# Optimization experiments

Measured on AMD Instinct MI355X. Metric: run time of the kernel, lower is better.

## Reference

```python
import math
import jax, jax.numpy as jnp
import numpy as np

N_NODES = 100000
N_EDGES = 1600000
IN_DIM = 512
HID = 128
OUT_DIM = 1
N_LAYERS = 8
ALPHA = 0.1
THETA = 0.5


def setup_inputs() -> dict:
    key = jax.random.key(0)
    ks = jax.random.split(key, 8)
    x = jax.random.normal(ks[0], (N_NODES, IN_DIM), dtype=jnp.float32)
    edge_index = jax.random.randint(ks[1], (2, N_EDGES), 0, N_NODES, dtype=jnp.int64)
    edge_weight = jax.random.uniform(ks[2], (N_EDGES,), dtype=jnp.float32)
    s_in = 1.0 / math.sqrt(IN_DIM)
    s_h = 1.0 / math.sqrt(HID)
    W_in = jax.random.uniform(ks[3], (IN_DIM, HID), jnp.float32, -s_in, s_in)
    b_in = jax.random.uniform(ks[4], (HID,), jnp.float32, -s_in, s_in)
    W_layers = jax.random.uniform(ks[5], (N_LAYERS, HID, HID), jnp.float32, -s_h, s_h)
    W_out = jax.random.uniform(ks[6], (HID, OUT_DIM), jnp.float32, -s_h, s_h)
    b_out = jax.random.uniform(ks[7], (OUT_DIM,), jnp.float32, -s_h, s_h)
    return {"x": x, "edge_index": edge_index, "edge_weight": edge_weight,
            "W_in": W_in, "b_in": b_in, "W_layers": W_layers,
            "W_out": W_out, "b_out": b_out}


def _gcn_norm(edge_index, n_nodes, dtype):
    # gcn_norm with add_self_loops=True and unit edge weights
    # (GCN2Net never forwards edge_weight into GCN2Conv).
    loop = jnp.arange(n_nodes, dtype=edge_index.dtype)
    src = jnp.concatenate([edge_index[0], loop])
    dst = jnp.concatenate([edge_index[1], loop])
    w = jnp.ones(src.shape[0], dtype=dtype)
    deg = jax.ops.segment_sum(w, dst, num_segments=n_nodes)
    dinv = jnp.where(deg > 0, jax.lax.rsqrt(deg), 0.0).astype(dtype)
    norm = dinv[src] * w * dinv[dst]
    return src, dst, norm


def reference(x, edge_index, edge_weight, W_in, b_in, W_layers, W_out, b_out):
    n = x.shape[0]
    src, dst, norm = _gcn_norm(edge_index, n, x.dtype)

    x = x @ W_in + b_in          # initial_proj: [N, HID]
    x0 = x
    for i in range(N_LAYERS):
        # sparse neighbor aggregation: A_hat @ x
        agg = jax.ops.segment_sum(x[src] * norm[:, None], dst, num_segments=n)
        # initial residual
        h = (1.0 - ALPHA) * agg + ALPHA * x0
        # identity mapping (shared_weights=True): (1-beta)*h + beta*(h @ W)
        beta = math.log(THETA / (i + 1) + 1.0)
        x = (1.0 - beta) * h + beta * (h @ W_layers[i])
        x = jax.nn.relu(x)
        # dropout omitted (eval mode / drop_prob=0)
    return x @ W_out + b_out     # final_proj: [N, OUT_DIM]
```

## Files before the change

### kernel.cpp

```cpp
#include <hip/hip_runtime.h>
#include <math.h>

#define NN 100000
#define NE 1600000
#define IN_DIM 512
#define HID 128
#define N_LAYERS 8
#define NB 98
#define PADMAX 2000000
#define NBUCK 391
#define BCAP2 4608
#define EPB 4096

typedef __attribute__((ext_vector_type(4))) float f32x4;
typedef __attribute__((ext_vector_type(8))) _Float16 h16x8;
typedef __attribute__((ext_vector_type(2))) _Float16 h16x2;


__global__ void deg_count_kernel(const int* __restrict__ dst, int* __restrict__ deg) {
    int e = blockIdx.x * blockDim.x + threadIdx.x;
    if (e < NE) atomicAdd(&deg[dst[e]], 1);
}

__global__ void dinv_kernel(const int* __restrict__ deg, float* __restrict__ dinv) {
    int i = blockIdx.x * blockDim.x + threadIdx.x;
    if (i < NN) dinv[i] = rsqrtf((float)(deg[i] + 1));
}

__global__ void scan1_kernel(const int* __restrict__ deg, int* __restrict__ bsum) {
    __shared__ int s[16];
    int gi = blockIdx.x * 1024 + threadIdx.x;
    int d = (gi < NN) ? deg[gi] : 0;
    int r = (d + 3) & ~3;
    for (int off = 32; off; off >>= 1) r += __shfl_down(r, off, 64);
    if ((threadIdx.x & 63) == 0) s[threadIdx.x >> 6] = r;
    __syncthreads();
    if (threadIdx.x == 0) {
        int t = 0;
        for (int i = 0; i < 16; ++i) t += s[i];
        bsum[blockIdx.x] = t;
    }
}

__global__ void scan2_kernel(const int* __restrict__ bsum, int* __restrict__ boff,
                             int* __restrict__ row_ptr) {
    __shared__ int s[128];
    int tid = threadIdx.x;
    int v = (tid < NB) ? bsum[tid] : 0;
    s[tid] = v;
    __syncthreads();
    for (int off = 1; off < 128; off <<= 1) {
        int t = (tid >= off) ? s[tid - off] : 0;
        __syncthreads();
        s[tid] += t;
        __syncthreads();
    }
    if (tid < NB) boff[tid] = s[tid] - v;
    if (tid == NB - 1) row_ptr[NN] = s[tid];
}

__global__ void scan3_kernel(const int* __restrict__ deg, const int* __restrict__ boff,
                             int* __restrict__ row_ptr, int* __restrict__ cursor) {
    __shared__ int s[1024];
    int tid = threadIdx.x;
    int gi = blockIdx.x * 1024 + tid;
    int d = (gi < NN) ? deg[gi] : 0;
    int v = (d + 3) & ~3;
    s[tid] = v;
    __syncthreads();
    for (int off = 1; off < 1024; off <<= 1) {
        int t = (tid >= off) ? s[tid - off] : 0;
        __syncthreads();
        s[tid] += t;
        __syncthreads();
    }
    if (gi < NN) {
        int o = boff[blockIdx.x] + s[tid] - v;
        row_ptr[gi] = o;
        cursor[gi]  = o;
    }
}

__global__ void pad_kernel(const int* __restrict__ deg, const int* __restrict__ row_ptr,
                           int* __restrict__ col) {
    int i = blockIdx.x * 256 + threadIdx.x;
    if (i < NN) {
        int d = deg[i];
        int s = row_ptr[i] + d;
        int e = row_ptr[i] + ((d + 3) & ~3);
        for (int p = s; p < e; ++p) col[p] = NN;
    }
}

__global__ __launch_bounds__(256) void bucket2_kernel(
    const int* __restrict__ src, const int* __restrict__ dst,
    int* __restrict__ bcnt, int2* __restrict__ pairs) {
    __shared__ int hist[NBUCK];
    __shared__ int scan_[NBUCK + 1];
    __shared__ int gb[NBUCK];
    __shared__ int curs[NBUCK];
    __shared__ int2 lp[EPB];
    int t = threadIdx.x;
    int e0 = blockIdx.x * EPB;
    int ne = NE - e0; if (ne > EPB) ne = EPB;

    for (int i = t; i < NBUCK; i += 256) hist[i] = 0;
    __syncthreads();
    for (int i = t; i < ne; i += 256)
        atomicAdd(&hist[dst[e0 + i] >> 8], 1);
    __syncthreads();

    if (t < 64) {
        int run = 0;
        for (int c = 0; c < 7; ++c) {
            int i = c * 64 + t;
            int h = (i < NBUCK) ? hist[i] : 0;
            int v = h;
            for (int off = 1; off < 64; off <<= 1) {
                int tmp = __shfl_up(v, off, 64);
                if (t >= off) v += tmp;
            }
            if (i < NBUCK) scan_[i] = run + v - h;
            run += __shfl(v, 63, 64);
        }
        if (t == 0) scan_[NBUCK] = run;
    }
    __syncthreads();

    for (int i = t; i < NBUCK; i += 256) {
        int h = hist[i];
        gb[i] = h ? atomicAdd(&bcnt[i], h) : 0;
        curs[i] = scan_[i];
    }
    __syncthreads();

    for (int i = t; i < ne; i += 256) {
        int d = dst[e0 + i], s = src[e0 + i];
        int slot = atomicAdd(&curs[d >> 8], 1);
        lp[slot] = make_int2(s, d);
    }
    __syncthreads();

    for (int i = t; i < ne; i += 256) {
        int lo = 0, hi = NBUCK;
        while (hi - lo > 1) {
            int mid = (lo + hi) >> 1;
            if (scan_[mid] <= i) lo = mid; else hi = mid;
        }
        pairs[(size_t)lo * BCAP2 + gb[lo] + (i - scan_[lo])] = lp[i];
    }
}

__global__ __launch_bounds__(512) void fill2_kernel(
    const int* __restrict__ bcnt, const int2* __restrict__ pairs,
    int* __restrict__ cursor, int* __restrict__ col) {
    int b = blockIdx.x;
    int n = bcnt[b];
    const int2* seg = pairs + (size_t)b * BCAP2;
#pragma unroll 4
    for (int i = threadIdx.x; i < n; i += 512) {
        int2 sd = seg[i];
        int pos = atomicAdd(&cursor[sd.y], 1);
        col[pos] = sd.x;
    }
}

__global__ void zero_sentinel_kernel(_Float16* __restrict__ a, _Float16* __restrict__ b) {
    int t = threadIdx.x;
    a[(size_t)NN * HID + t] = (_Float16)0.f;
    b[(size_t)NN * HID + t] = (_Float16)0.f;
}


__global__ void wprep_init_kernel(const float* __restrict__ W,
                                  _Float16* __restrict__ Bhi, _Float16* __restrict__ Blo) {
    int t = blockIdx.x * 256 + threadIdx.x;
    if (t >= 8 * 16 * 64) return;
    int lane = t & 63, nkk = t >> 6;
    int n = nkk >> 4, kk = nkk & 15;
    int scol = n * 16 + (lane & 15);
    int sr0 = kk * 32 + (lane >> 4) * 8;
#pragma unroll
    for (int j = 0; j < 8; ++j) {
        float w = W[(size_t)(sr0 + j) * HID + scol];
        _Float16 hi = (_Float16)w;
        _Float16 lo = (_Float16)(w - (float)hi);
        Bhi[(size_t)t * 8 + j] = hi;
        Blo[(size_t)t * 8 + j] = lo;
    }
}

__global__ void wprep_layers_kernel(const float* __restrict__ WL,
                                    _Float16* __restrict__ Bhi, _Float16* __restrict__ Blo) {
    int t = blockIdx.x * 256 + threadIdx.x;
    if (t >= N_LAYERS * 8 * 4 * 64) return;
    int layer = t >> 11;
    int r = t & 2047;
    int lane = r & 63, nkk = r >> 6;
    int n = nkk >> 2, kk = nkk & 3;
    const float* W = WL + (size_t)layer * HID * HID;
    int scol = n * 16 + (lane & 15);
    int sr0 = kk * 32 + (lane >> 4) * 8;
#pragma unroll
    for (int j = 0; j < 8; ++j) {
        float w = W[(size_t)(sr0 + j) * HID + scol];
        _Float16 hi = (_Float16)w;
        _Float16 lo = (_Float16)(w - (float)hi);
        Bhi[(size_t)t * 8 + j] = hi;
        Blo[(size_t)t * 8 + j] = lo;
    }
}


__device__ inline int xsw(int row, int blk) {
    return row * 512 + ((blk ^ (row & 7)) << 3);
}

__global__ __launch_bounds__(1024) void init_mfma_kernel(
    const float* __restrict__ x, const h16x8* __restrict__ Bhi, const h16x8* __restrict__ Blo,
    const float* __restrict__ b, const float* __restrict__ dinv,
    _Float16* __restrict__ ycur, _Float16* __restrict__ x0h) {
    __shared__ _Float16 xs[64 * 512];
    int t = threadIdx.x;
    int row0 = blockIdx.x * 64;

#pragma unroll
    for (int i = 0; i < 4; ++i) {
        int c = t + 1024 * i;
        int row = c >> 6, blk = c & 63;
        int grow = row0 + row; if (grow >= NN) grow = NN - 1;
        const float* p = x + (size_t)grow * IN_DIM + blk * 8;
        float4 v0 = *(const float4*)p;
        float4 v1 = *(const float4*)(p + 4);
        h16x8 h;
        h[0] = (_Float16)v0.x; h[1] = (_Float16)v0.y;
        h[2] = (_Float16)v0.z; h[3] = (_Float16)v0.w;
        h[4] = (_Float16)v1.x; h[5] = (_Float16)v1.y;
        h[6] = (_Float16)v1.z; h[7] = (_Float16)v1.w;
        *(h16x8*)&xs[xsw(row, blk)] = h;
    }
    __syncthreads();

    int lane = t & 63, wid = t >> 6;
    int nsel = wid & 7, mhalf = (wid >> 3) * 2;
    int rsel = lane & 15, ksel = lane >> 4;

    f32x4 acc[2];
#pragma unroll
    for (int m = 0; m < 2; ++m) acc[m] = (f32x4){0.f, 0.f, 0.f, 0.f};

#pragma unroll
    for (int kk = 0; kk < 16; ++kk) {
        h16x8 bh = Bhi[(nsel * 16 + kk) * 64 + lane];
        h16x8 bl = Blo[(nsel * 16 + kk) * 64 + lane];
#pragma unroll
        for (int m = 0; m < 2; ++m) {
            h16x8 a = *(const h16x8*)&xs[xsw((mhalf + m) * 16 + rsel, kk * 4 + ksel)];
            acc[m] = __builtin_amdgcn_mfma_f32_16x16x32_f16(a, bh, acc[m], 0, 0, 0);
            acc[m] = __builtin_amdgcn_mfma_f32_16x16x32_f16(a, bl, acc[m], 0, 0, 0);
        }
    }

    int col = nsel * 16 + rsel;
    float bias = b[col];
#pragma unroll
    for (int m = 0; m < 2; ++m) {
#pragma unroll
        for (int r = 0; r < 4; ++r) {
            int row = row0 + (mhalf + m) * 16 + ksel * 4 + r;
            if (row < NN) {
                float v = acc[m][r] + bias;
                float di = dinv[row];
                ycur[(size_t)row * HID + col] = (_Float16)(di * v);
                x0h[(size_t)row * HID + col]  = (_Float16)v;
            }
        }
    }
}


__device__ inline int hsw(int row, int blk) {
    return row * 128 + ((blk ^ (row & 7)) << 3);
}

__global__ __launch_bounds__(512) void fused_layer_kernel(
    const _Float16* __restrict__ y, const _Float16* __restrict__ x0,
    const int* __restrict__ row_ptr, const int* __restrict__ col,
    const float* __restrict__ dinv,
    const h16x8* __restrict__ Bhi, const h16x8* __restrict__ Blo,
    float beta, _Float16* __restrict__ yout) {
    __shared__ _Float16 hs[64 * 128];
    int t = threadIdx.x;
    int lane = t & 63, wid = t >> 6;
    int node0 = blockIdx.x * 64;
    int g = lane >> 4, q = lane & 15;

    h16x8 bh[4], bl[4];
#pragma unroll
    for (int kk = 0; kk < 4; ++kk) {
        bh[kk] = Bhi[(wid * 4 + kk) * 64 + lane];
        bl[kk] = Blo[(wid * 4 + kk) * 64 + lane];
    }

    const h16x8* x8 = (const h16x8*)y;
#pragma unroll
    for (int j = 0; j < 2; ++j) {
        int ln = wid * 8 + j * 4 + g;
        int node = node0 + ln;
        int valid = node < NN;
        int nd = valid ? node : 0;
        float di = dinv[nd];
        h16x8 sv = x8[(size_t)nd * 16 + q];
        h16x8 zv = ((const h16x8*)x0)[(size_t)nd * 16 + q];

        float acc[8];
#pragma unroll
        for (int jj = 0; jj < 8; ++jj) acc[jj] = 0.f;

        int p  = valid ? row_ptr[nd] : 0;
        int p1 = valid ? row_ptr[nd + 1] : 0;
#pragma unroll 2
        for (; p < p1; p += 4) {
            int4 c4 = *(const int4*)(col + p);
            h16x8 v0 = x8[(size_t)c4.x * 16 + q];
            h16x8 v1 = x8[(size_t)c4.y * 16 + q];
            h16x8 v2 = x8[(size_t)c4.z * 16 + q];
            h16x8 v3 = x8[(size_t)c4.w * 16 + q];
#pragma unroll
            for (int jj = 0; jj < 8; ++jj)
                acc[jj] += ((float)v0[jj] + (float)v1[jj])
                         + ((float)v2[jj] + (float)v3[jj]);
        }

        h16x8 o16;
#pragma unroll
        for (int jj = 0; jj < 8; ++jj) {
            float s = acc[jj] + (float)sv[jj];
            o16[jj] = (_Float16)(0.9f * (di * s) + 0.1f * (float)zv[jj]);
        }
        *(h16x8*)&hs[hsw(ln, q)] = o16;
    }
    __syncthreads();

    int rsel = lane & 15, ksel = lane >> 4;
    f32x4 acc[4];
#pragma unroll
    for (int m = 0; m < 4; ++m) acc[m] = (f32x4){0.f, 0.f, 0.f, 0.f};

#pragma unroll
    for (int m = 0; m < 4; ++m)
#pragma unroll
        for (int kk = 0; kk < 4; ++kk) {
            h16x8 a = *(const h16x8*)&hs[hsw(m * 16 + rsel, kk * 4 + ksel)];
            acc[m] = __builtin_amdgcn_mfma_f32_16x16x32_f16(a, bh[kk], acc[m], 0, 0, 0);
            acc[m] = __builtin_amdgcn_mfma_f32_16x16x32_f16(a, bl[kk], acc[m], 0, 0, 0);
        }

    float ob = 1.0f - beta;
    int colw = wid * 16 + rsel;
#pragma unroll
    for (int m = 0; m < 4; ++m) {
#pragma unroll
        for (int r = 0; r < 4; ++r) {
            int lr = m * 16 + ksel * 4 + r;
            int row = node0 + lr;
            if (row < NN) {
                float h = (float)hs[lr * 128 + (((colw >> 3) ^ (lr & 7)) << 3) + (colw & 7)];
                float v = ob * h + beta * acc[m][r];
                v = v > 0.f ? v : 0.f;
                yout[(size_t)row * HID + colw] = (_Float16)(dinv[row] * v);
            }
        }
    }
}


__global__ __launch_bounds__(256) void final16_kernel(
    const _Float16* __restrict__ y, const int* __restrict__ deg,
    const float* __restrict__ Wout, const float* __restrict__ bout,
    float* __restrict__ out) {
    int node = blockIdx.x * 4 + (threadIdx.x >> 6);
    int lane = threadIdx.x & 63;
    h16x2 a = ((const h16x2*)y)[(size_t)node * 64 + lane];
    float2 w = ((const float2*)Wout)[lane];
    float v = (float)a[0] * w.x + (float)a[1] * w.y;
#pragma unroll
    for (int off = 32; off; off >>= 1) v += __shfl_down(v, off, 64);
    if (lane == 0) out[node] = v * sqrtf((float)(deg[node] + 1)) + bout[0];
}


extern "C" void kernel_launch(void* const* d_in, const int* in_sizes, int n_in,
                              void* d_out, int out_size, void* d_ws, size_t ws_size,
                              hipStream_t stream) {
    const float* x_in     = (const float*)d_in[0];
    const int*   ei       = (const int*)d_in[1];
    const float* W_in     = (const float*)d_in[3];
    const float* b_in     = (const float*)d_in[4];
    const float* W_layers = (const float*)d_in[5];
    const float* W_out    = (const float*)d_in[6];
    const float* b_out    = (const float*)d_in[7];
    float* out = (float*)d_out;

    const int* src = ei;
    const int* dst = ei + NE;

    char* ws = (char*)d_ws;
    size_t off = 0;
    auto alloc = [&](size_t bytes) {
        size_t p = off;
        off = (off + bytes + 255) & ~(size_t)255;
        return p;
    };
    int*   deg     = (int*)(ws + alloc((size_t)NN * 4));
    float* dinv    = (float*)(ws + alloc((size_t)NN * 4));
    int*   row_ptr = (int*)(ws + alloc((size_t)(NN + 1) * 4));
    int*   cursor  = (int*)(ws + alloc((size_t)NN * 4));
    int*   bsum    = (int*)(ws + alloc((size_t)NB * 4));
    int*   boff    = (int*)(ws + alloc((size_t)NB * 4));
    int*   bcnt    = (int*)(ws + alloc((size_t)NBUCK * 4));
    int*   col     = (int*)(ws + alloc((size_t)PADMAX * 4));
    size_t x0_off  = alloc((size_t)NN * HID * 2);
    _Float16* x0h  = (_Float16*)(ws + x0_off);
    int2*  pairs   = (int2*)(ws + x0_off);
    _Float16* bufA = (_Float16*)(ws + alloc((size_t)(NN + 16) * HID * 2));
    _Float16* bufB = (_Float16*)(ws + alloc((size_t)(NN + 16) * HID * 2));
    _Float16* Bhi0 = (_Float16*)(ws + alloc((size_t)IN_DIM * HID * 2));
    _Float16* Blo0 = (_Float16*)(ws + alloc((size_t)IN_DIM * HID * 2));
    _Float16* BhiL = (_Float16*)(ws + alloc((size_t)N_LAYERS * HID * HID * 2));
    _Float16* BloL = (_Float16*)(ws + alloc((size_t)N_LAYERS * HID * HID * 2));

    hipMemsetAsync(deg, 0, (size_t)NN * 4, stream);
    hipMemsetAsync(bcnt, 0, (size_t)NBUCK * 4, stream);

    deg_count_kernel<<<NE / 256, 256, 0, stream>>>(dst, deg);
    dinv_kernel<<<(NN + 255) / 256, 256, 0, stream>>>(deg, dinv);
    scan1_kernel<<<NB, 1024, 0, stream>>>(deg, bsum);
    scan2_kernel<<<1, 128, 0, stream>>>(bsum, boff, row_ptr);
    scan3_kernel<<<NB, 1024, 0, stream>>>(deg, boff, row_ptr, cursor);
    pad_kernel<<<(NN + 255) / 256, 256, 0, stream>>>(deg, row_ptr, col);
    bucket2_kernel<<<(NE + EPB - 1) / EPB, 256, 0, stream>>>(src, dst, bcnt, pairs);
    fill2_kernel<<<NBUCK, 512, 0, stream>>>(bcnt, pairs, cursor, col);
    zero_sentinel_kernel<<<1, 128, 0, stream>>>(bufA, bufB);

    wprep_init_kernel<<<32, 256, 0, stream>>>(W_in, Bhi0, Blo0);
    wprep_layers_kernel<<<64, 256, 0, stream>>>(W_layers, BhiL, BloL);

    init_mfma_kernel<<<(NN + 63) / 64, 1024, 0, stream>>>(
        x_in, (const h16x8*)Bhi0, (const h16x8*)Blo0, b_in, dinv, bufA, x0h);

    _Float16* cur = bufA;
    _Float16* nxt = bufB;
    for (int l = 0; l < N_LAYERS; ++l) {
        float beta = logf(0.5f / (float)(l + 1) + 1.0f);
        fused_layer_kernel<<<(NN + 63) / 64, 512, 0, stream>>>(
            cur, x0h, row_ptr, col, dinv,
            (const h16x8*)(BhiL + (size_t)l * HID * HID),
            (const h16x8*)(BloL + (size_t)l * HID * HID), beta, nxt);
        _Float16* tmp = cur; cur = nxt; nxt = tmp;
    }

    final16_kernel<<<NN / 4, 256, 0, stream>>>(cur, deg, W_out, b_out, out);
}
```

Measured before the change: 947.3 us.

## Fold degree count, dinv, padding and sentinel zeroing into existing preprocessing kernels

Degree counting moves into the bucketing kernel, dinv is computed in scan3, column padding moves to the tail of fill2, and sentinel zeroing moves into scan2. This removes four kernel launches and one memset, plus a separate pass over the destination array. x0 is also pre-scaled by alpha so the per-layer residual blend saves a multiply. The cost is more global atomics inside the bucketing kernel, and fill2's padding loop relies on its block-to-node mapping, with each bucket covering 256 nodes.

```diff
diff --git a/kernel.cpp b/kernel.cpp
--- a/kernel.cpp
+++ b/kernel.cpp
@@ -17,84 +17,9 @@
 typedef __attribute__((ext_vector_type(2))) _Float16 h16x2;
 
 
-__global__ void deg_count_kernel(const int* __restrict__ dst, int* __restrict__ deg) {
-    int e = blockIdx.x * blockDim.x + threadIdx.x;
-    if (e < NE) atomicAdd(&deg[dst[e]], 1);
-}
-
-__global__ void dinv_kernel(const int* __restrict__ deg, float* __restrict__ dinv) {
-    int i = blockIdx.x * blockDim.x + threadIdx.x;
-    if (i < NN) dinv[i] = rsqrtf((float)(deg[i] + 1));
-}
-
-__global__ void scan1_kernel(const int* __restrict__ deg, int* __restrict__ bsum) {
-    __shared__ int s[16];
-    int gi = blockIdx.x * 1024 + threadIdx.x;
-    int d = (gi < NN) ? deg[gi] : 0;
-    int r = (d + 3) & ~3;
-    for (int off = 32; off; off >>= 1) r += __shfl_down(r, off, 64);
-    if ((threadIdx.x & 63) == 0) s[threadIdx.x >> 6] = r;
-    __syncthreads();
-    if (threadIdx.x == 0) {
-        int t = 0;
-        for (int i = 0; i < 16; ++i) t += s[i];
-        bsum[blockIdx.x] = t;
-    }
-}
-
-__global__ void scan2_kernel(const int* __restrict__ bsum, int* __restrict__ boff,
-                             int* __restrict__ row_ptr) {
-    __shared__ int s[128];
-    int tid = threadIdx.x;
-    int v = (tid < NB) ? bsum[tid] : 0;
-    s[tid] = v;
-    __syncthreads();
-    for (int off = 1; off < 128; off <<= 1) {
-        int t = (tid >= off) ? s[tid - off] : 0;
-        __syncthreads();
-        s[tid] += t;
-        __syncthreads();
-    }
-    if (tid < NB) boff[tid] = s[tid] - v;
-    if (tid == NB - 1) row_ptr[NN] = s[tid];
-}
-
-__global__ void scan3_kernel(const int* __restrict__ deg, const int* __restrict__ boff,
-                             int* __restrict__ row_ptr, int* __restrict__ cursor) {
-    __shared__ int s[1024];
-    int tid = threadIdx.x;
-    int gi = blockIdx.x * 1024 + tid;
-    int d = (gi < NN) ? deg[gi] : 0;
-    int v = (d + 3) & ~3;
-    s[tid] = v;
-    __syncthreads();
-    for (int off = 1; off < 1024; off <<= 1) {
-        int t = (tid >= off) ? s[tid - off] : 0;
-        __syncthreads();
-        s[tid] += t;
-        __syncthreads();
-    }
-    if (gi < NN) {
-        int o = boff[blockIdx.x] + s[tid] - v;
-        row_ptr[gi] = o;
-        cursor[gi]  = o;
-    }
-}
-
-__global__ void pad_kernel(const int* __restrict__ deg, const int* __restrict__ row_ptr,
-                           int* __restrict__ col) {
-    int i = blockIdx.x * 256 + threadIdx.x;
-    if (i < NN) {
-        int d = deg[i];
-        int s = row_ptr[i] + d;
-        int e = row_ptr[i] + ((d + 3) & ~3);
-        for (int p = s; p < e; ++p) col[p] = NN;
-    }
-}
-
 __global__ __launch_bounds__(256) void bucket2_kernel(
     const int* __restrict__ src, const int* __restrict__ dst,
-    int* __restrict__ bcnt, int2* __restrict__ pairs) {
+    int* __restrict__ deg, int* __restrict__ bcnt, int2* __restrict__ pairs) {
     __shared__ int hist[NBUCK];
     __shared__ int scan_[NBUCK + 1];
     __shared__ int gb[NBUCK];
@@ -106,8 +31,11 @@
 
     for (int i = t; i < NBUCK; i += 256) hist[i] = 0;
     __syncthreads();
-    for (int i = t; i < ne; i += 256)
-        atomicAdd(&hist[dst[e0 + i] >> 8], 1);
+    for (int i = t; i < ne; i += 256) {
+        int d = dst[e0 + i];
+        atomicAdd(&hist[d >> 8], 1);
+        atomicAdd(&deg[d], 1);
+    }
     __syncthreads();
 
     if (t < 64) {
@@ -151,9 +79,69 @@
     }
 }
 
+__global__ void scan1_kernel(const int* __restrict__ deg, int* __restrict__ bsum) {
+    __shared__ int s[16];
+    int gi = blockIdx.x * 1024 + threadIdx.x;
+    int d = (gi < NN) ? deg[gi] : 0;
+    int r = (d + 3) & ~3;
+    for (int off = 32; off; off >>= 1) r += __shfl_down(r, off, 64);
+    if ((threadIdx.x & 63) == 0) s[threadIdx.x >> 6] = r;
+    __syncthreads();
+    if (threadIdx.x == 0) {
+        int t = 0;
+        for (int i = 0; i < 16; ++i) t += s[i];
+        bsum[blockIdx.x] = t;
+    }
+}
+
+__global__ void scan2_kernel(const int* __restrict__ bsum, int* __restrict__ boff,
+                             int* __restrict__ row_ptr,
+                             _Float16* __restrict__ sa, _Float16* __restrict__ sb) {
+    __shared__ int s[128];
+    int tid = threadIdx.x;
+    sa[(size_t)NN * HID + tid] = (_Float16)0.f;
+    sb[(size_t)NN * HID + tid] = (_Float16)0.f;
+    int v = (tid < NB) ? bsum[tid] : 0;
+    s[tid] = v;
+    __syncthreads();
+    for (int off = 1; off < 128; off <<= 1) {
+        int t = (tid >= off) ? s[tid - off] : 0;
+        __syncthreads();
+        s[tid] += t;
+        __syncthreads();
+    }
+    if (tid < NB) boff[tid] = s[tid] - v;
+    if (tid == NB - 1) row_ptr[NN] = s[tid];
+}
+
+__global__ void scan3_kernel(const int* __restrict__ deg, const int* __restrict__ boff,
+                             int* __restrict__ row_ptr, int* __restrict__ cursor,
+                             float* __restrict__ dinv) {
+    __shared__ int s[1024];
+    int tid = threadIdx.x;
+    int gi = blockIdx.x * 1024 + tid;
+    int d = (gi < NN) ? deg[gi] : 0;
+    int v = (d + 3) & ~3;
+    s[tid] = v;
+    __syncthreads();
+    for (int off = 1; off < 1024; off <<= 1) {
+        int t = (tid >= off) ? s[tid - off] : 0;
+        __syncthreads();
+        s[tid] += t;
+        __syncthreads();
+    }
+    if (gi < NN) {
+        int o = boff[blockIdx.x] + s[tid] - v;
+        row_ptr[gi] = o;
+        cursor[gi]  = o;
+        dinv[gi]    = rsqrtf((float)(d + 1));
+    }
+}
+
 __global__ __launch_bounds__(512) void fill2_kernel(
     const int* __restrict__ bcnt, const int2* __restrict__ pairs,
-    int* __restrict__ cursor, int* __restrict__ col) {
+    const int* __restrict__ row_ptr, int* __restrict__ cursor,
+    int* __restrict__ col) {
     int b = blockIdx.x;
     int n = bcnt[b];
     const int2* seg = pairs + (size_t)b * BCAP2;
@@ -163,12 +151,15 @@
         int pos = atomicAdd(&cursor[sd.y], 1);
         col[pos] = sd.x;
     }
-}
-
-__global__ void zero_sentinel_kernel(_Float16* __restrict__ a, _Float16* __restrict__ b) {
-    int t = threadIdx.x;
-    a[(size_t)NN * HID + t] = (_Float16)0.f;
-    b[(size_t)NN * HID + t] = (_Float16)0.f;
+    __syncthreads();
+    int d0 = b * 256;
+    int d1 = d0 + 256; if (d1 > NN) d1 = NN;
+    for (int d = d0 + threadIdx.x; d < d1; d += 512) {
+        int rp  = row_ptr[d];
+        int end = cursor[d];
+        int pend = rp + ((end - rp + 3) & ~3);
+        for (int p = end; p < pend; ++p) col[p] = NN;
+    }
 }
 
 
@@ -272,7 +263,7 @@
                 float v = acc[m][r] + bias;
                 float di = dinv[row];
                 ycur[(size_t)row * HID + col] = (_Float16)(di * v);
-                x0h[(size_t)row * HID + col]  = (_Float16)v;
+                x0h[(size_t)row * HID + col]  = (_Float16)(0.1f * v);
             }
         }
     }
@@ -332,11 +323,12 @@
                          + ((float)v2[jj] + (float)v3[jj]);
         }
 
+        float d9 = 0.9f * di;
         h16x8 o16;
 #pragma unroll
         for (int jj = 0; jj < 8; ++jj) {
             float s = acc[jj] + (float)sv[jj];
-            o16[jj] = (_Float16)(0.9f * (di * s) + 0.1f * (float)zv[jj]);
+            o16[jj] = (_Float16)(d9 * s + (float)zv[jj]);
         }
         *(h16x8*)&hs[hsw(ln, q)] = o16;
     }
@@ -413,12 +405,12 @@
         return p;
     };
     int*   deg     = (int*)(ws + alloc((size_t)NN * 4));
+    int*   bcnt    = (int*)(ws + alloc((size_t)NBUCK * 4));
     float* dinv    = (float*)(ws + alloc((size_t)NN * 4));
     int*   row_ptr = (int*)(ws + alloc((size_t)(NN + 1) * 4));
     int*   cursor  = (int*)(ws + alloc((size_t)NN * 4));
     int*   bsum    = (int*)(ws + alloc((size_t)NB * 4));
     int*   boff    = (int*)(ws + alloc((size_t)NB * 4));
-    int*   bcnt    = (int*)(ws + alloc((size_t)NBUCK * 4));
     int*   col     = (int*)(ws + alloc((size_t)PADMAX * 4));
     size_t x0_off  = alloc((size_t)NN * HID * 2);
     _Float16* x0h  = (_Float16*)(ws + x0_off);
@@ -430,18 +422,13 @@
     _Float16* BhiL = (_Float16*)(ws + alloc((size_t)N_LAYERS * HID * HID * 2));
     _Float16* BloL = (_Float16*)(ws + alloc((size_t)N_LAYERS * HID * HID * 2));
 
-    hipMemsetAsync(deg, 0, (size_t)NN * 4, stream);
-    hipMemsetAsync(bcnt, 0, (size_t)NBUCK * 4, stream);
-
-    deg_count_kernel<<<NE / 256, 256, 0, stream>>>(dst, deg);
-    dinv_kernel<<<(NN + 255) / 256, 256, 0, stream>>>(deg, dinv);
+    hipMemsetAsync(deg, 0, (size_t)((char*)bcnt - (char*)deg) + (size_t)NBUCK * 4, stream);
+
+    bucket2_kernel<<<(NE + EPB - 1) / EPB, 256, 0, stream>>>(src, dst, deg, bcnt, pairs);
     scan1_kernel<<<NB, 1024, 0, stream>>>(deg, bsum);
-    scan2_kernel<<<1, 128, 0, stream>>>(bsum, boff, row_ptr);
-    scan3_kernel<<<NB, 1024, 0, stream>>>(deg, boff, row_ptr, cursor);
-    pad_kernel<<<(NN + 255) / 256, 256, 0, stream>>>(deg, row_ptr, col);
-    bucket2_kernel<<<(NE + EPB - 1) / EPB, 256, 0, stream>>>(src, dst, bcnt, pairs);
-    fill2_kernel<<<NBUCK, 512, 0, stream>>>(bcnt, pairs, cursor, col);
-    zero_sentinel_kernel<<<1, 128, 0, stream>>>(bufA, bufB);
+    scan2_kernel<<<1, 128, 0, stream>>>(bsum, boff, row_ptr, bufA, bufB);
+    scan3_kernel<<<NB, 1024, 0, stream>>>(deg, boff, row_ptr, cursor, dinv);
+    fill2_kernel<<<NBUCK, 512, 0, stream>>>(bcnt, pairs, row_ptr, cursor, col);
 
     wprep_init_kernel<<<32, 256, 0, stream>>>(W_in, Bhi0, Blo0);
     wprep_layers_kernel<<<64, 256, 0, stream>>>(W_layers, BhiL, BloL);
```

Result: faster. 897.6 us (-5.3%).
